# Kernel optimization log

Measured on AMD Instinct MI355X. Metric: run time of the kernel, lower is better.

Reference implementation:

```python
import jax, jax.numpy as jnp
from jax import lax
import numpy as np

MIN_WIDTH, MAX_WIDTH, NUM_TEMPLATES = 10, 40, 4
# torch.linspace(10, 40, 4, dtype=int) -> [10, 20, 30, 40]
WIDTHS = [int(w) for w in np.linspace(MIN_WIDTH, MAX_WIDTH, NUM_TEMPLATES)]
B, L = 64, 65536


def setup_inputs() -> dict:
    key = jax.random.key(0)
    k1, _ = jax.random.split(key)
    x = jax.random.normal(k1, (B, L), dtype=jnp.float32)
    template_weights = jnp.ones((NUM_TEMPLATES,), dtype=jnp.float32)
    return {"x": x, "template_weights": template_weights}


def _hann_corr(x, width):
    """Zero-padded cross-correlation of x [B, L] with hanning(2*width).

    Equivalent to the original triple loop: out[b, j] = sum_k x[b, j-width+k] * hann[k],
    k in [0, 2*width), out-of-range signal entries treated as zero. Asymmetric
    padding (width, width-1) yields exactly L outputs matching positions j=0..L-1.
    """
    templ = jnp.asarray(np.hanning(2 * width), dtype=jnp.float32)
    out = lax.conv_general_dilated(
        x[:, None, :],                 # [B, 1, L]
        templ[None, None, :],          # [1, 1, 2w]
        window_strides=(1,),
        padding=[(width, width - 1)],
        dimension_numbers=("NCH", "OIH", "NCH"),
    )
    return out[:, 0, :]                # [B, L]


def reference(x, template_weights):
    # [B, T, L] correlation maps, one per template width
    corr_maps = jnp.stack([_hann_corr(x, w) for w in WIDTHS], axis=1)
    weights = jax.nn.softmax(template_weights)          # [T]
    return jnp.sum(corr_maps * weights[None, :, None], axis=1)  # [B, L]
```

## Files before the change

kernel.cpp:

```cpp
#include <hip/hip_runtime.h>
#include <math.h>

#define BLOCK 256
#define OPT 8
#define TILE (BLOCK * OPT)
#define HALO 48
#define NF 80
#define LDSX4 (TILE / 4 + 2 * HALO / 4)
#define PHYS4(i) ((i) + ((i) >> 3))
#define LDSP4 (LDSX4 + LDSX4 / 8 + 2)

typedef float nfloat4 __attribute__((ext_vector_type(4)));

__global__ __launch_bounds__(BLOCK) void hann_fir_kernel(
    const float* __restrict__ x, const float* __restrict__ tw,
    float* __restrict__ out, int Ln)
{
    __shared__ float4 xs4[LDSP4];
    __shared__ float Fs[NF];

    const int tid = threadIdx.x;
    const int tiles_per_row = Ln / TILE;
    const int row = blockIdx.x / tiles_per_row;
    const int tile = blockIdx.x - row * tiles_per_row;
    const long long row_base = (long long)row * Ln;
    const int tile_start = tile * TILE;

    if (tid < NF) {
        float t0 = tw[0], t1 = tw[1], t2 = tw[2], t3 = tw[3];
        float m = fmaxf(fmaxf(t0, t1), fmaxf(t2, t3));
        float e0 = expf(t0 - m), e1 = expf(t1 - m);
        float e2 = expf(t2 - m), e3 = expf(t3 - m);
        float inv = 1.0f / (e0 + e1 + e2 + e3);
        float wts[4] = {e0 * inv, e1 * inv, e2 * inv, e3 * inv};
        float f = 0.0f;
        #pragma unroll
        for (int t = 0; t < 4; ++t) {
            int w = 10 * (t + 1);
            int k = tid - 40 + w;
            if (k >= 0 && k < 2 * w) {
                float h = 0.5f - 0.5f * cosf(6.28318530717958647692f *
                                             (float)k / (float)(2 * w - 1));
                f += wts[t] * h;
            }
        }
        Fs[tid] = f;
    }

    for (int i4 = tid; i4 < LDSX4; i4 += BLOCK) {
        int j = tile_start - HALO + 4 * i4;
        float4 v;
        if (j >= 0 && j + 3 < Ln) {
            v = *reinterpret_cast<const float4*>(x + row_base + j);
        } else {
            v.x = (j + 0 >= 0 && j + 0 < Ln) ? x[row_base + j + 0] : 0.0f;
            v.y = (j + 1 >= 0 && j + 1 < Ln) ? x[row_base + j + 1] : 0.0f;
            v.z = (j + 2 >= 0 && j + 2 < Ln) ? x[row_base + j + 2] : 0.0f;
            v.w = (j + 3 >= 0 && j + 3 < Ln) ? x[row_base + j + 3] : 0.0f;
        }
        xs4[PHYS4(i4)] = v;
    }
    __syncthreads();

    float acc[OPT];
    #pragma unroll
    for (int r = 0; r < OPT; ++r) acc[r] = 0.0f;

    const float4* Fs4 = reinterpret_cast<const float4*>(Fs);
    const int b4 = 2 * tid + (HALO - 40) / 4;

    float4 c0 = xs4[PHYS4(b4)];
    float4 c1 = xs4[PHYS4(b4 + 1)];
    #pragma unroll
    for (int g = 0; g < NF / 4; ++g) {
        float4 c2 = xs4[PHYS4(b4 + g + 2)];
        float4 f = Fs4[g];
        float win[12] = {c0.x, c0.y, c0.z, c0.w,
                         c1.x, c1.y, c1.z, c1.w,
                         c2.x, c2.y, c2.z, c2.w};
        #pragma unroll
        for (int r = 0; r < OPT; ++r) {
            acc[r] = fmaf(f.x, win[r + 0], acc[r]);
            acc[r] = fmaf(f.y, win[r + 1], acc[r]);
            acc[r] = fmaf(f.z, win[r + 2], acc[r]);
            acc[r] = fmaf(f.w, win[r + 3], acc[r]);
        }
        c0 = c1; c1 = c2;
    }

    const long long o = row_base + tile_start + OPT * tid;
    nfloat4 o0 = {acc[0], acc[1], acc[2], acc[3]};
    nfloat4 o1 = {acc[4], acc[5], acc[6], acc[7]};
    __builtin_nontemporal_store(o0, reinterpret_cast<nfloat4*>(out + o));
    __builtin_nontemporal_store(o1, reinterpret_cast<nfloat4*>(out + o + 4));
}

extern "C" void kernel_launch(void* const* d_in, const int* in_sizes, int n_in,
                              void* d_out, int out_size, void* d_ws, size_t ws_size,
                              hipStream_t stream) {
    const float* x  = (const float*)d_in[0];
    const float* tw = (const float*)d_in[1];
    float* out = (float*)d_out;

    const int B = 64;
    const int L = 65536;
    (void)in_sizes; (void)n_in; (void)out_size; (void)d_ws; (void)ws_size;

    const int tiles_per_row = L / TILE;
    dim3 grid(B * tiles_per_row);
    dim3 block(BLOCK);
    hann_fir_kernel<<<grid, block, 0, stream>>>(x, tw, out, L);
}
```

Baseline: 75.56 us.

## Use persistent blocks with register-prefetched next tile to overlap loads and compute

Replaces the one-tile-per-block grid with a fixed grid of 512 persistent blocks that loop over tiles. While computing the current tile from LDS, each thread prefetches the next tile's input into registers and writes it to LDS at the start of the next iteration. The aim is to hide global load latency and cut block launch and filter setup overhead. In exchange it adds register pressure and an extra barrier per tile, and with 2048 tiles each block handles only four, so there is little pipelining depth.

```diff
diff --git a/kernel.cpp b/kernel.cpp
--- a/kernel.cpp
+++ b/kernel.cpp
@@ -6,25 +6,40 @@
 #define TILE (BLOCK * OPT)
 #define HALO 48
 #define NF 80
+#define LJ 65536
+#define BATCH 64
+#define TPR (LJ / TILE)
+#define NTILES (BATCH * TPR)
+#define GRID 512
 #define LDSX4 (TILE / 4 + 2 * HALO / 4)
 #define PHYS4(i) ((i) + ((i) >> 3))
 #define LDSP4 (LDSX4 + LDSX4 / 8 + 2)
+#define R2CNT (LDSX4 - 2 * BLOCK)
 
 typedef float nfloat4 __attribute__((ext_vector_type(4)));
 
+__device__ __forceinline__ float4 load_guard(const float* __restrict__ x,
+                                             long long rb, int j) {
+    float4 v;
+    if (j >= 0 && j + 3 < LJ) {
+        v = *reinterpret_cast<const float4*>(x + rb + j);
+    } else {
+        v.x = (j + 0 >= 0 && j + 0 < LJ) ? x[rb + j + 0] : 0.0f;
+        v.y = (j + 1 >= 0 && j + 1 < LJ) ? x[rb + j + 1] : 0.0f;
+        v.z = (j + 2 >= 0 && j + 2 < LJ) ? x[rb + j + 2] : 0.0f;
+        v.w = (j + 3 >= 0 && j + 3 < LJ) ? x[rb + j + 3] : 0.0f;
+    }
+    return v;
+}
+
 __global__ __launch_bounds__(BLOCK) void hann_fir_kernel(
     const float* __restrict__ x, const float* __restrict__ tw,
-    float* __restrict__ out, int Ln)
+    float* __restrict__ out)
 {
     __shared__ float4 xs4[LDSP4];
     __shared__ float Fs[NF];
 
     const int tid = threadIdx.x;
-    const int tiles_per_row = Ln / TILE;
-    const int row = blockIdx.x / tiles_per_row;
-    const int tile = blockIdx.x - row * tiles_per_row;
-    const long long row_base = (long long)row * Ln;
-    const int tile_start = tile * TILE;
 
     if (tid < NF) {
         float t0 = tw[0], t1 = tw[1], t2 = tw[2], t3 = tw[3];
@@ -47,52 +62,72 @@
         Fs[tid] = f;
     }
 
-    for (int i4 = tid; i4 < LDSX4; i4 += BLOCK) {
-        int j = tile_start - HALO + 4 * i4;
-        float4 v;
-        if (j >= 0 && j + 3 < Ln) {
-            v = *reinterpret_cast<const float4*>(x + row_base + j);
-        } else {
-            v.x = (j + 0 >= 0 && j + 0 < Ln) ? x[row_base + j + 0] : 0.0f;
-            v.y = (j + 1 >= 0 && j + 1 < Ln) ? x[row_base + j + 1] : 0.0f;
-            v.z = (j + 2 >= 0 && j + 2 < Ln) ? x[row_base + j + 2] : 0.0f;
-            v.w = (j + 3 >= 0 && j + 3 < Ln) ? x[row_base + j + 3] : 0.0f;
-        }
-        xs4[PHYS4(i4)] = v;
-    }
-    __syncthreads();
-
-    float acc[OPT];
-    #pragma unroll
-    for (int r = 0; r < OPT; ++r) acc[r] = 0.0f;
-
     const float4* Fs4 = reinterpret_cast<const float4*>(Fs);
     const int b4 = 2 * tid + (HALO - 40) / 4;
 
-    float4 c0 = xs4[PHYS4(b4)];
-    float4 c1 = xs4[PHYS4(b4 + 1)];
-    #pragma unroll
-    for (int g = 0; g < NF / 4; ++g) {
-        float4 c2 = xs4[PHYS4(b4 + g + 2)];
-        float4 f = Fs4[g];
-        float win[12] = {c0.x, c0.y, c0.z, c0.w,
-                         c1.x, c1.y, c1.z, c1.w,
-                         c2.x, c2.y, c2.z, c2.w};
-        #pragma unroll
-        for (int r = 0; r < OPT; ++r) {
-            acc[r] = fmaf(f.x, win[r + 0], acc[r]);
-            acc[r] = fmaf(f.y, win[r + 1], acc[r]);
-            acc[r] = fmaf(f.z, win[r + 2], acc[r]);
-            acc[r] = fmaf(f.w, win[r + 3], acc[r]);
-        }
-        c0 = c1; c1 = c2;
+    int tau = blockIdx.x;
+    float4 r0, r1, r2;
+    {
+        int row = tau / TPR, tc = tau - row * TPR;
+        long long rb = (long long)row * LJ;
+        int ts = tc * TILE - HALO;
+        r0 = load_guard(x, rb, ts + 4 * tid);
+        r1 = load_guard(x, rb, ts + 4 * (tid + BLOCK));
+        if (tid < R2CNT) r2 = load_guard(x, rb, ts + 4 * (tid + 2 * BLOCK));
     }
 
-    const long long o = row_base + tile_start + OPT * tid;
-    nfloat4 o0 = {acc[0], acc[1], acc[2], acc[3]};
-    nfloat4 o1 = {acc[4], acc[5], acc[6], acc[7]};
-    __builtin_nontemporal_store(o0, reinterpret_cast<nfloat4*>(out + o));
-    __builtin_nontemporal_store(o1, reinterpret_cast<nfloat4*>(out + o + 4));
+    while (tau < NTILES) {
+        const int row = tau / TPR, tc = tau - row * TPR;
+        const long long rb = (long long)row * LJ;
+        const int ts = tc * TILE;
+        const int tnext = tau + GRID;
+
+        __syncthreads();
+        xs4[PHYS4(tid)] = r0;
+        xs4[PHYS4(tid + BLOCK)] = r1;
+        if (tid < R2CNT) xs4[PHYS4(tid + 2 * BLOCK)] = r2;
+        __syncthreads();
+
+        if (tnext < NTILES) {
+            int nrow = tnext / TPR, ntc = tnext - nrow * TPR;
+            long long nrb = (long long)nrow * LJ;
+            int nts = ntc * TILE - HALO;
+            r0 = load_guard(x, nrb, nts + 4 * tid);
+            r1 = load_guard(x, nrb, nts + 4 * (tid + BLOCK));
+            if (tid < R2CNT) r2 = load_guard(x, nrb, nts + 4 * (tid + 2 * BLOCK));
+        }
+
+        float acc[OPT];
+        #pragma unroll
+        for (int r = 0; r < OPT; ++r) acc[r] = 0.0f;
+
+        float4 c0 = xs4[PHYS4(b4)];
+        float4 c1 = xs4[PHYS4(b4 + 1)];
+        #pragma unroll
+        for (int g = 0; g < NF / 4; ++g) {
+            float4 c2 = xs4[PHYS4(b4 + g + 2)];
+            float4 f = Fs4[g];
+            float win[12] = {c0.x, c0.y, c0.z, c0.w,
+                             c1.x, c1.y, c1.z, c1.w,
+                             c2.x, c2.y, c2.z, c2.w};
+            #pragma unroll
+            for (int r = 0; r < OPT; ++r) {
+                acc[r] = fmaf(f.x, win[r + 0], acc[r]);
+                acc[r] = fmaf(f.y, win[r + 1], acc[r]);
+                acc[r] = fmaf(f.z, win[r + 2], acc[r]);
+                acc[r] = fmaf(f.w, win[r + 3], acc[r]);
+            }
+            c0 = c1; c1 = c2;
+        }
+
+        const long long o = rb + ts + OPT * tid;
+        nfloat4 o0 = {acc[0], acc[1], acc[2], acc[3]};
+        nfloat4 o1 = {acc[4], acc[5], acc[6], acc[7]};
+        __builtin_nontemporal_store(o0, reinterpret_cast<nfloat4*>(out + o));
+        __builtin_nontemporal_store(o1, reinterpret_cast<nfloat4*>(out + o + 4));
+
+        tau = tnext;
+    }
 }
 
 extern "C" void kernel_launch(void* const* d_in, const int* in_sizes, int n_in,
@@ -101,13 +136,7 @@
     const float* x  = (const float*)d_in[0];
     const float* tw = (const float*)d_in[1];
     float* out = (float*)d_out;
-
-    const int B = 64;
-    const int L = 65536;
     (void)in_sizes; (void)n_in; (void)out_size; (void)d_ws; (void)ws_size;
 
-    const int tiles_per_row = L / TILE;
-    dim3 grid(B * tiles_per_row);
-    dim3 block(BLOCK);
-    hann_fir_kernel<<<grid, block, 0, stream>>>(x, tw, out, L);
+    hann_fir_kernel<<<dim3(GRID), dim3(BLOCK), 0, stream>>>(x, tw, out);
 }
```

Result: slower. 78.34 us (+3.7%).
